# Optimization experiments

Hardware: AMD Instinct MI355X
Metric: run time of the kernel (lower is better)

Reference implementation:

```python
import jax, jax.numpy as jnp
import numpy as np

H, W, D_F, N, BINS = 64, 64, 768, 16, 16
SPAN = 1.0
CLIP = 3.0


def _make_bin_idx(h, w, bins):
    # torch _fftfreq_1d == np.fft.fftfreq (k/n with negative wrap)
    fx = np.fft.fftfreq(h).astype(np.float32)
    fy = np.fft.fftfreq(w).astype(np.float32)
    r = np.sqrt(fx[:, None] ** 2 + fy[None, :] ** 2)  # (h, w)
    edges = np.linspace(r.min(), r.max() + 1e-12, bins + 1, dtype=np.float32)
    # torch.bucketize(r, edges[1:-1], right=False) == searchsorted side='left'
    idx = np.searchsorted(edges[1:-1], r, side='left')
    return np.clip(idx, 0, bins - 1).astype(np.int32)


def setup_inputs() -> dict:
    key = jax.random.key(0)
    x = jax.random.normal(key, (N, D_F, H, W), dtype=jnp.float32)
    # parameter init exactly as torch __init__ (bins>1, span>0 branch)
    g_init = np.linspace(-SPAN, SPAN, BINS, dtype=np.float32)
    deltas = np.clip(g_init[1:] - g_init[:-1], 1e-6, None)
    raw_deltas = np.log(np.expm1(deltas)).astype(np.float32)  # inverse softplus
    g1 = np.float32(g_init[0])
    bin_idx_2d = _make_bin_idx(H, W, BINS)
    return {
        "x": x,
        "g1": jnp.asarray(g1),
        "raw_deltas": jnp.asarray(raw_deltas),
        "bin_idx_2d": jnp.asarray(bin_idx_2d),
    }


def _sqrt_lambda(g1, raw_deltas, bin_idx_2d):
    # monotone bin values g_b = g1 + cumsum(softplus(raw_deltas))
    deltas = jax.nn.softplus(raw_deltas)
    g = jnp.concatenate([g1[None], g1[None] + jnp.cumsum(deltas)], axis=0)  # (bins,)
    ell = g[bin_idx_2d]                      # (h, w) log-lambda per frequency
    ell = ell - ell.mean()                   # logdet gauge centering
    ell = jnp.clip(ell, -CLIP, CLIP)
    lam = jnp.exp(ell)
    # logdet gauge: normalize geometric mean to 1 (clip may break centering)
    lam = lam / jnp.maximum(jnp.exp(jnp.log(lam).mean()), 1e-12)
    return jnp.sqrt(lam)


def reference(x, g1, raw_deltas, bin_idx_2d):
    sqrt_lam = _sqrt_lambda(g1, raw_deltas, bin_idx_2d).astype(x.dtype)
    X = jnp.fft.fft2(x, norm="ortho")                    # (n, d_f, h, w) complex
    y = jnp.fft.ifft2(X * sqrt_lam[None, None, :, :], norm="ortho").real
    return y.astype(x.dtype)
```

## Files before the change

kernel.cpp:

```cpp
#include <hip/hip_runtime.h>
#include <math.h>


__device__ __forceinline__ float2 cadd(float2 a, float2 b){ return make_float2(a.x+b.x, a.y+b.y); }
__device__ __forceinline__ float2 csub(float2 a, float2 b){ return make_float2(a.x-b.x, a.y-b.y); }
__device__ __forceinline__ float2 cmul(float2 a, float2 b){ return make_float2(a.x*b.x - a.y*b.y, a.x*b.y + a.y*b.x); }
__device__ __forceinline__ float2 cmulc(float2 a, float2 b){
  return make_float2(a.x*b.x + a.y*b.y, a.y*b.x - a.x*b.y);
}

template<int SGN>
__device__ __forceinline__ float2 crot(float2 a){
  return (SGN < 0) ? make_float2(a.y, -a.x) : make_float2(-a.y, a.x);
}

template<int SGN>
__device__ __forceinline__ void fft8(float2 a[8]){
  const float s = 0.70710678118654752440f;
  float2 e0=a[0], e1=a[2], e2=a[4], e3=a[6];
  float2 o0=a[1], o1=a[3], o2=a[5], o3=a[7];
  float2 t0=cadd(e0,e2), t1=csub(e0,e2), t2=cadd(e1,e3), t3=crot<SGN>(csub(e1,e3));
  float2 E0=cadd(t0,t2), E2=csub(t0,t2), E1=cadd(t1,t3), E3=csub(t1,t3);
  float2 u0=cadd(o0,o2), u1=csub(o0,o2), u2=cadd(o1,o3), u3=crot<SGN>(csub(o1,o3));
  float2 O0=cadd(u0,u2), O2=csub(u0,u2), O1=cadd(u1,u3), O3=csub(u1,u3);
  const float2 w1 = make_float2( s, (SGN < 0) ? -s : s);
  const float2 w3 = make_float2(-s, (SGN < 0) ? -s : s);
  O1 = cmul(O1, w1);
  O2 = crot<SGN>(O2);
  O3 = cmul(O3, w3);
  a[0]=cadd(E0,O0); a[4]=csub(E0,O0);
  a[1]=cadd(E1,O1); a[5]=csub(E1,O1);
  a[2]=cadd(E2,O2); a[6]=csub(E2,O2);
  a[3]=cadd(E3,O3); a[7]=csub(E3,O3);
}

__device__ __forceinline__ void lds_sync(){
  __builtin_amdgcn_fence(__ATOMIC_ACQ_REL, "wavefront");
  __builtin_amdgcn_wave_barrier();
  __builtin_amdgcn_fence(__ATOMIC_ACQ_REL, "wavefront");
}

__global__ void filter_kernel(const float* __restrict__ g1p,
                              const float* __restrict__ rawd,
                              const int*   __restrict__ bidx,
                              float*       __restrict__ Sperm){
  __shared__ float gsh[16];
  __shared__ float red[256];
  const int tid = threadIdx.x;
  if (tid == 0){
    float g = g1p[0];
    gsh[0] = g;
    for (int b = 0; b < 15; ++b){
      float d = rawd[b];
      float sp = (d > 20.f) ? d : log1pf(expf(d));
      g += sp;
      gsh[b+1] = g;
    }
  }
  __syncthreads();
  float ell[16];
  float sacc = 0.f;
  #pragma unroll
  for (int i = 0; i < 16; ++i){
    int p = tid + 256*i;
    ell[i] = gsh[bidx[p]];
    sacc += ell[i];
  }
  red[tid] = sacc; __syncthreads();
  for (int off = 128; off > 0; off >>= 1){
    if (tid < off) red[tid] += red[tid + off];
    __syncthreads();
  }
  float mean1 = red[0] * (1.f/4096.f);
  __syncthreads();
  sacc = 0.f;
  #pragma unroll
  for (int i = 0; i < 16; ++i){
    float e = ell[i] - mean1;
    e = fminf(fmaxf(e, -3.f), 3.f);
    ell[i] = e;
    sacc += e;
  }
  red[tid] = sacc; __syncthreads();
  for (int off = 128; off > 0; off >>= 1){
    if (tid < off) red[tid] += red[tid + off];
    __syncthreads();
  }
  float mean2 = red[0] * (1.f/4096.f);
  #pragma unroll
  for (int i = 0; i < 16; ++i){
    int p = tid + 256*i;
    int h = p >> 6, w = p & 63;
    float val = expf(0.5f * (ell[i] - mean2)) * (1.0f/4096.0f);
    int pw = ((w & 7) << 3) | (w >> 3);
    Sperm[h*64 + pw] = val;
  }
}

__global__ __launch_bounds__(512, 4) void spectral_kernel(
    const float* __restrict__ x, const float* __restrict__ Sp, float* __restrict__ y)
{
  __shared__ float2 tile[64*66];
  float4* tile4 = reinterpret_cast<float4*>(tile);
  const int tid = threadIdx.x;
  const int g = tid >> 3;
  const int t = tid & 7;
  const long long baseA = (long long)blockIdx.x * 8192;
  const float* xA = x + baseA;
  const float* xB = xA + 4096;
  float* yA = y + baseA;
  float* yB = yA + 4096;

  float2 tw[8];
  #pragma unroll
  for (int j = 0; j < 8; ++j){
    float sv, cv;
    __sincosf(-(float)M_PI * (float)(t*j) / 32.0f, &sv, &cv);
    tw[j] = make_float2(cv, sv);
  }

  {
    const float* rA = xA + (g << 6);
    const float* rB = xB + (g << 6);
    float2 a[8];
    #pragma unroll
    for (int j = 0; j < 8; ++j) a[j] = make_float2(rA[t + 8*j], rB[t + 8*j]);
    fft8<-1>(a);
    #pragma unroll
    for (int j = 1; j < 8; ++j) a[j] = cmul(a[j], tw[j]);
    #pragma unroll
    for (int q = 0; q < 4; ++q)
      tile4[33*g + 4*t + q] = make_float4(a[2*q].x, a[2*q].y, a[2*q+1].x, a[2*q+1].y);
    lds_sync();
    #pragma unroll
    for (int j = 0; j < 8; ++j) a[j] = tile[66*g + 8*j + t];
    fft8<-1>(a);
    lds_sync();
    #pragma unroll
    for (int q = 0; q < 4; ++q)
      tile4[33*g + 4*t + q] = make_float4(a[2*q].x, a[2*q].y, a[2*q+1].x, a[2*q+1].y);
  }
  __syncthreads();

  {
    const int c = g;
    const int d = c & 7, Wv = c >> 3;
    float2 a[8];
    #pragma unroll
    for (int j = 0; j < 8; ++j) a[j] = tile[66*(t + 8*j) + c];
    fft8<-1>(a);
    #pragma unroll
    for (int j = 1; j < 8; ++j) a[j] = cmul(a[j], tw[j]);
    lds_sync();
    #pragma unroll
    for (int q = 0; q < 4; ++q)
      tile4[33*(8*t + d) + 4*Wv + q] = make_float4(a[2*q].x, a[2*q].y, a[2*q+1].x, a[2*q+1].y);
    lds_sync();
    #pragma unroll
    for (int j = 0; j < 8; ++j) a[j] = tile[66*(8*j + d) + 8*Wv + t];
    fft8<-1>(a);
    #pragma unroll
    for (int j = 0; j < 8; ++j){
      float f = Sp[((t + 8*j) << 6) + c];
      a[j].x *= f; a[j].y *= f;
    }
    fft8<+1>(a);
    #pragma unroll
    for (int j = 1; j < 8; ++j) a[j] = cmulc(a[j], tw[j]);
    lds_sync();
    #pragma unroll
    for (int q = 0; q < 4; ++q)
      tile4[33*(8*t + d) + 4*Wv + q] = make_float4(a[2*q].x, a[2*q].y, a[2*q+1].x, a[2*q+1].y);
    lds_sync();
    #pragma unroll
    for (int j = 0; j < 8; ++j) a[j] = tile[66*(8*j + d) + 8*Wv + t];
    fft8<+1>(a);
    lds_sync();
    #pragma unroll
    for (int j = 0; j < 8; ++j) tile[66*(t + 8*j) + c] = a[j];
  }
  __syncthreads();

  {
    float2 a[8];
    #pragma unroll
    for (int q = 0; q < 4; ++q){
      float4 v = tile4[33*g + 4*t + q];
      a[2*q]   = make_float2(v.x, v.y);
      a[2*q+1] = make_float2(v.z, v.w);
    }
    fft8<+1>(a);
    #pragma unroll
    for (int j = 1; j < 8; ++j) a[j] = cmulc(a[j], tw[j]);
    lds_sync();
    #pragma unroll
    for (int q = 0; q < 4; ++q)
      tile4[33*g + 4*t + q] = make_float4(a[2*q].x, a[2*q].y, a[2*q+1].x, a[2*q+1].y);
    lds_sync();
    #pragma unroll
    for (int j = 0; j < 8; ++j) a[j] = tile[66*g + 8*j + t];
    fft8<+1>(a);
    float* wA = yA + (g << 6) + t;
    float* wB = yB + (g << 6) + t;
    #pragma unroll
    for (int j = 0; j < 8; ++j){ wA[8*j] = a[j].x; wB[8*j] = a[j].y; }
  }
}

extern "C" void kernel_launch(void* const* d_in, const int* in_sizes, int n_in,
                              void* d_out, int out_size, void* d_ws, size_t ws_size,
                              hipStream_t stream){
  (void)in_sizes; (void)n_in; (void)out_size; (void)ws_size;
  const float* x    = (const float*)d_in[0];
  const float* g1   = (const float*)d_in[1];
  const float* rawd = (const float*)d_in[2];
  const int*   bidx = (const int*)d_in[3];
  float* y     = (float*)d_out;
  float* Sperm = (float*)d_ws;

  filter_kernel<<<dim3(1), dim3(256), 0, stream>>>(g1, rawd, bidx, Sperm);
  spectral_kernel<<<dim3(6144), dim3(512), 0, stream>>>(x, Sperm, y);
}
```

Measured before the change: 359.2 us.

## Remap thread-to-data indices to cut LDS bank conflicts and twiddle cost

Changes how threads in each wavefront map to FFT rows and columns. The row passes use a layout where lanes differ in row within a group, and the column passes use a bit-permuted sub-index with swapped float4 halves, aiming to reduce LDS bank conflicts and improve global access patterns. Twiddles are now built by recurrence from one sincos instead of eight, and the launch bound asks for 8 blocks per SM, which may force register spilling. The added index arithmetic and the permuted stores risk correctness if the mapping is wrong.

```diff
diff --git a/kernel.cpp b/kernel.cpp
--- a/kernel.cpp
+++ b/kernel.cpp
@@ -40,6 +40,15 @@
   __builtin_amdgcn_fence(__ATOMIC_ACQ_REL, "wavefront");
 }
 
+__device__ __forceinline__ void build_tw(int t, float2 tw[8]){
+  float sv, cv;
+  __sincosf(-(float)M_PI * (float)t / 32.0f, &sv, &cv);
+  const float2 wstep = make_float2(cv, sv);
+  tw[0] = make_float2(1.f, 0.f);
+  #pragma unroll
+  for (int j = 1; j < 8; ++j) tw[j] = cmul(tw[j-1], wstep);
+}
+
 __global__ void filter_kernel(const float* __restrict__ g1p,
                               const float* __restrict__ rawd,
                               const int*   __restrict__ bidx,
@@ -97,14 +106,22 @@
   }
 }
 
-__global__ __launch_bounds__(512, 4) void spectral_kernel(
+__global__ __launch_bounds__(512, 8) void spectral_kernel(
     const float* __restrict__ x, const float* __restrict__ Sp, float* __restrict__ y)
 {
   __shared__ float2 tile[64*66];
   float4* tile4 = reinterpret_cast<float4*>(tile);
   const int tid = threadIdx.x;
-  const int g = tid >> 3;
-  const int t = tid & 7;
+  const int wv = tid >> 6;
+  const int l  = tid & 63;
+  const int o  = l & 7;
+  const int u  = l >> 3;
+  const int g  = (wv << 3) + o;
+  const int tA = u;
+  const int c  = (wv << 3) + o;
+  const int tB = ((u & 1) << 2) | (u & 2) | (u >> 2);
+  const int mB = (tB < 4) ? tB : (tB ^ 1);
+
   const long long baseA = (long long)blockIdx.x * 8192;
   const float* xA = x + baseA;
   const float* xB = xA + 4096;
@@ -112,80 +129,81 @@
   float* yB = yA + 4096;
 
   float2 tw[8];
-  #pragma unroll
-  for (int j = 0; j < 8; ++j){
-    float sv, cv;
-    __sincosf(-(float)M_PI * (float)(t*j) / 32.0f, &sv, &cv);
-    tw[j] = make_float2(cv, sv);
-  }
-
+
+  build_tw(tA, tw);
   {
     const float* rA = xA + (g << 6);
     const float* rB = xB + (g << 6);
     float2 a[8];
     #pragma unroll
-    for (int j = 0; j < 8; ++j) a[j] = make_float2(rA[t + 8*j], rB[t + 8*j]);
+    for (int j = 0; j < 8; ++j) a[j] = make_float2(rA[tA + 8*j], rB[tA + 8*j]);
     fft8<-1>(a);
     #pragma unroll
     for (int j = 1; j < 8; ++j) a[j] = cmul(a[j], tw[j]);
     #pragma unroll
     for (int q = 0; q < 4; ++q)
-      tile4[33*g + 4*t + q] = make_float4(a[2*q].x, a[2*q].y, a[2*q+1].x, a[2*q+1].y);
-    lds_sync();
-    #pragma unroll
-    for (int j = 0; j < 8; ++j) a[j] = tile[66*g + 8*j + t];
+      tile4[33*g + 4*tA + q] = make_float4(a[2*q].x, a[2*q].y, a[2*q+1].x, a[2*q+1].y);
+    lds_sync();
+    #pragma unroll
+    for (int j = 0; j < 8; ++j) a[j] = tile[66*g + 8*j + tA];
     fft8<-1>(a);
     lds_sync();
     #pragma unroll
     for (int q = 0; q < 4; ++q)
-      tile4[33*g + 4*t + q] = make_float4(a[2*q].x, a[2*q].y, a[2*q+1].x, a[2*q+1].y);
-  }
-  __syncthreads();
-
-  {
-    const int c = g;
-    const int d = c & 7, Wv = c >> 3;
-    float2 a[8];
-    #pragma unroll
-    for (int j = 0; j < 8; ++j) a[j] = tile[66*(t + 8*j) + c];
-    fft8<-1>(a);
-    #pragma unroll
-    for (int j = 1; j < 8; ++j) a[j] = cmul(a[j], tw[j]);
-    lds_sync();
-    #pragma unroll
-    for (int q = 0; q < 4; ++q)
-      tile4[33*(8*t + d) + 4*Wv + q] = make_float4(a[2*q].x, a[2*q].y, a[2*q+1].x, a[2*q+1].y);
-    lds_sync();
-    #pragma unroll
-    for (int j = 0; j < 8; ++j) a[j] = tile[66*(8*j + d) + 8*Wv + t];
-    fft8<-1>(a);
-    #pragma unroll
-    for (int j = 0; j < 8; ++j){
-      float f = Sp[((t + 8*j) << 6) + c];
-      a[j].x *= f; a[j].y *= f;
-    }
-    fft8<+1>(a);
-    #pragma unroll
-    for (int j = 1; j < 8; ++j) a[j] = cmulc(a[j], tw[j]);
-    lds_sync();
-    #pragma unroll
-    for (int q = 0; q < 4; ++q)
-      tile4[33*(8*t + d) + 4*Wv + q] = make_float4(a[2*q].x, a[2*q].y, a[2*q+1].x, a[2*q+1].y);
-    lds_sync();
-    #pragma unroll
-    for (int j = 0; j < 8; ++j) a[j] = tile[66*(8*j + d) + 8*Wv + t];
-    fft8<+1>(a);
-    lds_sync();
-    #pragma unroll
-    for (int j = 0; j < 8; ++j) tile[66*(t + 8*j) + c] = a[j];
-  }
-  __syncthreads();
-
+      tile4[33*g + 4*tA + q] = make_float4(a[2*q].x, a[2*q].y, a[2*q+1].x, a[2*q+1].y);
+  }
+  __syncthreads();
+
+  build_tw(tB, tw);
   {
     float2 a[8];
     #pragma unroll
+    for (int j = 0; j < 8; ++j) a[j] = tile[66*(tB + 8*j) + c];
+    fft8<-1>(a);
+    #pragma unroll
+    for (int j = 1; j < 8; ++j) a[j] = cmul(a[j], tw[j]);
+    lds_sync();
+    #pragma unroll
     for (int q = 0; q < 4; ++q){
-      float4 v = tile4[33*g + 4*t + q];
+      float2 lo = a[2*q], hi = a[2*q+1];
+      if (q >= 2){ float2 t2 = lo; lo = hi; hi = t2; }
+      tile4[33*(8*tB + o) + 4*wv + q] = make_float4(lo.x, lo.y, hi.x, hi.y);
+    }
+    lds_sync();
+    #pragma unroll
+    for (int j = 0; j < 8; ++j) a[j] = tile[66*(8*j + o) + 8*wv + mB];
+    fft8<-1>(a);
+    #pragma unroll
+    for (int j = 0; j < 8; ++j){
+      float f = Sp[((tB + 8*j) << 6) + c];
+      a[j].x *= f; a[j].y *= f;
+    }
+    fft8<+1>(a);
+    #pragma unroll
+    for (int j = 1; j < 8; ++j) a[j] = cmulc(a[j], tw[j]);
+    lds_sync();
+    #pragma unroll
+    for (int q = 0; q < 4; ++q){
+      float2 lo = a[2*q], hi = a[2*q+1];
+      if (q >= 2){ float2 t2 = lo; lo = hi; hi = t2; }
+      tile4[33*(8*tB + o) + 4*wv + q] = make_float4(lo.x, lo.y, hi.x, hi.y);
+    }
+    lds_sync();
+    #pragma unroll
+    for (int j = 0; j < 8; ++j) a[j] = tile[66*(8*j + o) + 8*wv + mB];
+    fft8<+1>(a);
+    lds_sync();
+    #pragma unroll
+    for (int j = 0; j < 8; ++j) tile[66*(tB + 8*j) + c] = a[j];
+  }
+  __syncthreads();
+
+  build_tw(tA, tw);
+  {
+    float2 a[8];
+    #pragma unroll
+    for (int q = 0; q < 4; ++q){
+      float4 v = tile4[33*g + 4*tA + q];
       a[2*q]   = make_float2(v.x, v.y);
       a[2*q+1] = make_float2(v.z, v.w);
     }
@@ -195,15 +213,15 @@
     lds_sync();
     #pragma unroll
     for (int q = 0; q < 4; ++q)
-      tile4[33*g + 4*t + q] = make_float4(a[2*q].x, a[2*q].y, a[2*q+1].x, a[2*q+1].y);
-    lds_sync();
-    #pragma unroll
-    for (int j = 0; j < 8; ++j) a[j] = tile[66*g + 8*j + t];
-    fft8<+1>(a);
-    float* wA = yA + (g << 6) + t;
-    float* wB = yB + (g << 6) + t;
-    #pragma unroll
-    for (int j = 0; j < 8; ++j){ wA[8*j] = a[j].x; wB[8*j] = a[j].y; }
+      tile4[33*g + 4*tA + q] = make_float4(a[2*q].x, a[2*q].y, a[2*q+1].x, a[2*q+1].y);
+    lds_sync();
+    #pragma unroll
+    for (int j = 0; j < 8; ++j) a[j] = tile[66*g + 8*j + tA];
+    fft8<+1>(a);
+    float* pA = yA + (g << 6) + tA;
+    float* pB = yB + (g << 6) + tA;
+    #pragma unroll
+    for (int j = 0; j < 8; ++j){ pA[8*j] = a[j].x; pB[8*j] = a[j].y; }
   }
 }
 
```

New measurement: 396.7 us. 10.4% more time.
